# Performance work log

Measured on AMD Instinct MI355X. Metric: run time of the kernel, lower is better.

The kernel has to match this reference:

```python
import jax, jax.numpy as jnp
import numpy as np

N, E, G = 50000, 800000, 512
F, DE, DG = 64, 16, 32
H, HEADS, C, L, NC = 128, 4, 32, 3, 1
EPS = 1e-5


def _bn(x, g, b, m, v):
    # eval-mode BatchNorm1d with running stats
    return (x - m) / jnp.sqrt(v + EPS) * g + b


def setup_inputs():
    key = jax.random.key(0)
    ks = jax.random.split(key, 24)

    def bn_params(k, d):
        k1, k2, k3, k4 = jax.random.split(k, 4)
        return (1.0 + 0.1 * jax.random.normal(k1, (d,), jnp.float32),
                0.1 * jax.random.normal(k2, (d,), jnp.float32),
                0.1 * jax.random.normal(k3, (d,), jnp.float32),
                jax.random.uniform(k4, (d,), jnp.float32, 0.5, 1.5))

    sc = lambda k, sh, fan: jax.random.normal(k, sh, jnp.float32) / np.float32(np.sqrt(fan))
    inp = {}
    inp['x'] = jax.random.normal(ks[0], (N, F), jnp.float32)
    inp['edge_attr'] = jax.random.normal(ks[1], (E, DE), jnp.float32)
    inp['global_features'] = jax.random.normal(ks[2], (G, DG), jnp.float32)
    inp['edge_index'] = jax.random.randint(ks[3], (2, E), 0, N)
    inp['batch'] = jnp.sort(jax.random.randint(ks[4], (N,), 0, G))
    inp['node_w'] = sc(ks[5], (F, H), F); inp['node_b'] = jnp.zeros((H,), jnp.float32)
    inp['node_bn_g'], inp['node_bn_b'], inp['node_bn_m'], inp['node_bn_v'] = bn_params(ks[6], H)
    inp['edge_w'] = sc(ks[7], (DE, H), DE); inp['edge_b'] = jnp.zeros((H,), jnp.float32)
    inp['glob_w'] = sc(ks[8], (DG, H), DG); inp['glob_b'] = jnp.zeros((H,), jnp.float32)
    inp['glob_bn_g'], inp['glob_bn_b'], inp['glob_bn_m'], inp['glob_bn_v'] = bn_params(ks[9], H)
    inp['gat_lin'] = sc(ks[10], (L, H, HEADS * C), H)
    inp['gat_asrc'] = sc(ks[11], (L, HEADS, C), C)
    inp['gat_adst'] = sc(ks[12], (L, HEADS, C), C)
    inp['gat_bias'] = jnp.zeros((L, H), jnp.float32)
    bg, bb, bm, bv = zip(*[bn_params(jax.random.fold_in(ks[13], i), H) for i in range(L)])
    inp['bn_g'] = jnp.stack(bg); inp['bn_b'] = jnp.stack(bb)
    inp['bn_m'] = jnp.stack(bm); inp['bn_v'] = jnp.stack(bv)
    inp['lin1_w'] = sc(ks[14], (3 * H, H), 3 * H); inp['lin1_b'] = jnp.zeros((H,), jnp.float32)
    inp['lin2_w'] = sc(ks[15], (H, NC), H); inp['lin2_b'] = jnp.zeros((NC,), jnp.float32)
    return inp


def reference(x, edge_attr, global_features, edge_index, batch, node_w, node_b, node_bn_g, node_bn_b, node_bn_m, node_bn_v, edge_w, edge_b, glob_w, glob_b, glob_bn_g, glob_bn_b, glob_bn_m, glob_bn_v, gat_lin, gat_asrc, gat_adst, gat_bias, bn_g, bn_b, bn_m, bn_v, lin1_w, lin1_b, lin2_w, lin2_b):
    n = x.shape[0]
    h = jax.nn.relu(_bn(x @ node_w + node_b, node_bn_g, node_bn_b, node_bn_m, node_bn_v))
    _ = jax.nn.relu(edge_attr @ edge_w + edge_b)  # edge encoder: computed but unused by GATConv, as in source
    # add self loops (PyG GATConv default)
    loops = jnp.arange(n)
    src = jnp.concatenate([edge_index[0], loops])
    dst = jnp.concatenate([edge_index[1], loops])
    for i in range(L):
        identity = h
        hh = (h @ gat_lin[i]).reshape(n, HEADS, C)
        a_src = jnp.einsum('nhc,hc->nh', hh, gat_asrc[i])
        a_dst = jnp.einsum('nhc,hc->nh', hh, gat_adst[i])
        e = jax.nn.leaky_relu(a_src[src] + a_dst[dst], 0.2)  # [E+n, HEADS]
        e_max = jax.ops.segment_max(e, dst, num_segments=n)
        ee = jnp.exp(e - e_max[dst])
        den = jax.ops.segment_sum(ee, dst, num_segments=n)
        alpha = ee / (den[dst] + 1e-16)
        out = jax.ops.segment_sum(hh[src] * alpha[..., None], dst, num_segments=n)
        out = out.reshape(n, HEADS * C) + gat_bias[i]
        out = jax.nn.relu(_bn(out, bn_g[i], bn_b[i], bn_m[i], bn_v[i]))
        h = out + identity  # residual: dims always match (HEADS*C == H)
    g = global_features.shape[0]
    cnt = jax.ops.segment_sum(jnp.ones((n,), h.dtype), batch, num_segments=g)
    x_mean = jax.ops.segment_sum(h, batch, num_segments=g) / jnp.maximum(cnt, 1.0)[:, None]
    x_max = jax.ops.segment_max(h, batch, num_segments=g)
    x_max = jnp.where(jnp.isfinite(x_max), x_max, 0.0)  # guard rare empty graphs
    gfeat = jax.nn.relu(_bn(global_features @ glob_w + glob_b, glob_bn_g, glob_bn_b, glob_bn_m, glob_bn_v))
    z = jnp.concatenate([x_mean, x_max, gfeat], axis=1)
    z = jax.nn.relu(z @ lin1_w + lin1_b)
    return z @ lin2_w + lin2_b
```

## Files before the change

### kernel.cpp

```cpp
#include <hip/hip_runtime.h>
#include <hip/hip_bf16.h>

typedef unsigned short u16;
typedef unsigned int   u32;
typedef unsigned long long u64;

#define HD 128
#define FD 64
#define EPS 1e-5f
#define BSH 8
#define CAP 8192
#define TILE 2048

using bf16x8 = __attribute__((ext_vector_type(8))) short;
using f32x4  = __attribute__((ext_vector_type(4))) float;

__device__ __forceinline__ float b2f(u16 v) { return __uint_as_float(((u32)v) << 16); }
__device__ __forceinline__ u16 f2b(float f) {
    u32 u = __float_as_uint(f);
    return (u16)((u + 0x7FFF + ((u >> 16) & 1)) >> 16);
}
__device__ __forceinline__ float lo16(u32 u) { return __uint_as_float(u << 16); }
__device__ __forceinline__ float hi16(u32 u) { return __uint_as_float(u & 0xFFFF0000u); }

__global__ __launch_bounds__(256) void k_prep(
    const float* __restrict__ node_w, const float* __restrict__ gat_lin,
    u16* __restrict__ wf_node, u16* __restrict__ wf_gat,
    const int* __restrict__ batch, int* __restrict__ gs,
    int* __restrict__ zbase, int zn, int N, int G) {
    int y = blockIdx.y;
    int tid = threadIdx.x;
    if (y < 4) {
        const float* src; u16* dst; int K;
        if (y == 0) { src = node_w; dst = wf_node; K = FD; }
        else { src = gat_lin + (size_t)(y - 1) * HD * HD; dst = wf_gat + (size_t)(y - 1) * HD * HD; K = HD; }
        int KT = K >> 5;
        int total = K * HD;
        for (int f = blockIdx.x * 256 + tid; f < total; f += gridDim.x * 256) {
            int j = f & 7;
            int lane = (f >> 3) & 63;
            int t = f >> 9;
            int kt = t % KT;
            int ct = t / KT;
            int k = kt * 32 + (lane >> 4) * 8 + j;
            int col = ct * 16 + (lane & 15);
            dst[f] = f2b(src[k * HD + col]);
        }
    } else if (y == 4) {
        int i = blockIdx.x * 256 + tid;
        if (i < N) {
            int b = batch[i];
            if (i == 0) { for (int g = 0; g <= b; g++) gs[g] = 0; }
            else {
                int pb = batch[i - 1];
                for (int g = pb + 1; g <= b; g++) gs[g] = i;
            }
            if (i == N - 1) { for (int g = b + 1; g <= G; g++) gs[g] = N; }
        }
    } else {
        for (int i = blockIdx.x * 256 + tid; i < zn; i += gridDim.x * 256) zbase[i] = 0;
    }
}

__global__ __launch_bounds__(256) void k_binA_node(
    const int* __restrict__ src, const int* __restrict__ dst,
    int* __restrict__ bcur, u64* __restrict__ arena,
    const float* __restrict__ x, const u16* __restrict__ wf, const float* __restrict__ bias,
    const float* __restrict__ g, const float* __restrict__ bb, const float* __restrict__ m,
    const float* __restrict__ v, u16* __restrict__ h,
    int E, int NB, int numTiles, int N) {
    __shared__ __align__(16) char smem[TILE * 8 + 4 * 256 * 4];
    int tid = threadIdx.x;
    if ((int)blockIdx.x < numTiles) {
        u32* os   = (u32*)smem;
        u32* od   = os + TILE;
        int* hist = (int*)(od + TILE);
        int* obas = hist + 256;
        int* ofs  = obas + 256;
        int* gpos = ofs + 256;
        int base = blockIdx.x * TILE;
        int cntE = E - base; if (cntE > TILE) cntE = TILE;
        hist[tid] = 0;
        __syncthreads();
        u32 rs[TILE / 256], rd[TILE / 256];
        #pragma unroll
        for (int r = 0; r < TILE / 256; r++) {
            int li = r * 256 + tid;
            if (li < cntE) {
                rs[r] = src[base + li];
                rd[r] = dst[base + li];
                atomicAdd(&hist[rd[r] >> BSH], 1);
            }
        }
        __syncthreads();
        if (tid < 64) {
            int h0 = hist[4 * tid], h1 = hist[4 * tid + 1];
            int h2 = hist[4 * tid + 2], h3 = hist[4 * tid + 3];
            int s01 = h0 + h1;
            int loc = s01 + h2 + h3;
            int inc = loc;
            #pragma unroll
            for (int off = 1; off < 64; off <<= 1) {
                int tv = __shfl_up(inc, off);
                if (tid >= off) inc += tv;
            }
            int excl = inc - loc;
            obas[4 * tid] = excl;                 ofs[4 * tid] = excl;
            obas[4 * tid + 1] = excl + h0;        ofs[4 * tid + 1] = excl + h0;
            obas[4 * tid + 2] = excl + s01;       ofs[4 * tid + 2] = excl + s01;
            obas[4 * tid + 3] = excl + s01 + h2;  ofs[4 * tid + 3] = excl + s01 + h2;
        }
        __syncthreads();
        #pragma unroll
        for (int r = 0; r < TILE / 256; r++) {
            int li = r * 256 + tid;
            if (li < cntE) {
                int b = rd[r] >> BSH;
                int posn = atomicAdd(&ofs[b], 1);
                os[posn] = rs[r];
                od[posn] = rd[r];
            }
        }
        __syncthreads();
        if (tid < NB && hist[tid] > 0)
            gpos[tid] = atomicAdd(&bcur[tid], hist[tid]);
        __syncthreads();
        for (int li = tid; li < cntE; li += 256) {
            u32 d = od[li];
            int b = d >> BSH;
            int p = gpos[b] + (li - obas[b]);
            if (p < CAP) arena[(size_t)b * CAP + p] = ((u64)d << 32) | os[li];
        }
    } else {
        int nb = blockIdx.x - numTiles;
        int wv = tid >> 6, lane = tid & 63;
        int rowbase = nb * 64 + wv * 16;
        if (rowbase >= N) return;
        int n16 = lane & 15, quad = lane >> 4;
        int arow = min(rowbase + n16, N - 1);
        f32x4 acc[8] = {};
        #pragma unroll
        for (int kt = 0; kt < 2; kt++) {
            const float4* xp = (const float4*)(x + (size_t)arow * FD + kt * 32 + quad * 8);
            float4 a0 = xp[0], a1 = xp[1];
            bf16x8 a;
            a[0] = (short)f2b(a0.x); a[1] = (short)f2b(a0.y);
            a[2] = (short)f2b(a0.z); a[3] = (short)f2b(a0.w);
            a[4] = (short)f2b(a1.x); a[5] = (short)f2b(a1.y);
            a[6] = (short)f2b(a1.z); a[7] = (short)f2b(a1.w);
            #pragma unroll
            for (int ct = 0; ct < 8; ct++) {
                bf16x8 b = *(const bf16x8*)(wf + ((size_t)(ct * 2 + kt) * 64 + lane) * 8);
                acc[ct] = __builtin_amdgcn_mfma_f32_16x16x32_bf16(a, b, acc[ct], 0, 0, 0);
            }
        }
        #pragma unroll
        for (int ct = 0; ct < 8; ct++) {
            int col = ct * 16 + n16;
            float sc = g[col] * rsqrtf(v[col] + EPS);
            float bi = (bias[col] - m[col]) * sc + bb[col];
            #pragma unroll
            for (int reg = 0; reg < 4; reg++) {
                int row = rowbase + quad * 4 + reg;
                if (row < N) h[(size_t)row * HD + col] = f2b(fmaxf(acc[ct][reg] * sc + bi, 0.f));
            }
        }
    }
}

__global__ __launch_bounds__(256) void k_scanS(const int* __restrict__ bcur, int* __restrict__ bbase, int NB) {
    __shared__ int s[256];
    int tid = threadIdx.x;
    int v = (tid < NB) ? bcur[tid] : 0;
    s[tid] = v;
    __syncthreads();
    for (int off = 1; off < 256; off <<= 1) {
        int t = (tid >= off) ? s[tid - off] : 0;
        __syncthreads();
        s[tid] += t;
        __syncthreads();
    }
    if (tid < NB) bbase[tid] = s[tid] - v;
}

__global__ __launch_bounds__(256) void k_binB2(
    const int* __restrict__ bbase, const int* __restrict__ bcur,
    const u64* __restrict__ arena, int* __restrict__ rowptr, int* __restrict__ colidx,
    int N, int E) {
    __shared__ int rowL[256], lofs[256];
    int b = blockIdx.x, tid = threadIdx.x;
    int n0 = b << BSH;
    int n = n0 + tid;
    int nedge = bcur[b];
    if (nedge > CAP) nedge = CAP;
    lofs[tid] = 0;
    __syncthreads();
    for (int i = tid; i < nedge; i += 256) {
        int d = (int)(arena[(size_t)b * CAP + i] >> 32);
        atomicAdd(&lofs[d - n0], 1);
    }
    __syncthreads();
    rowL[tid] = lofs[tid];
    __syncthreads();
    if (tid < 64) {
        int h0 = rowL[4 * tid], h1 = rowL[4 * tid + 1];
        int h2 = rowL[4 * tid + 2], h3 = rowL[4 * tid + 3];
        int s01 = h0 + h1;
        int loc = s01 + h2 + h3;
        int inc = loc;
        #pragma unroll
        for (int off = 1; off < 64; off <<= 1) {
            int tv = __shfl_up(inc, off);
            if (tid >= off) inc += tv;
        }
        int excl = inc - loc;
        rowL[4 * tid] = excl;
        rowL[4 * tid + 1] = excl + h0;
        rowL[4 * tid + 2] = excl + s01;
        rowL[4 * tid + 3] = excl + s01 + h2;
    }
    __syncthreads();
    int base = bbase[b];
    if (n < N) rowptr[n] = base + rowL[tid];
    if (b == 0 && tid == 0) rowptr[N] = E;
    rowL[tid] += base;
    lofs[tid] = 0;
    __syncthreads();
    for (int i = tid; i < nedge; i += 256) {
        u64 pk = arena[(size_t)b * CAP + i];
        int d = (int)(pk >> 32), s = (int)(pk & 0xFFFFFFFFu);
        int slot = atomicAdd(&lofs[d - n0], 1);
        colidx[rowL[d - n0] + slot] = s;
    }
}

__global__ __launch_bounds__(256) void k_gat_mfma(
    const u16* __restrict__ h, const u16* __restrict__ wf,
    const float* __restrict__ asrcw, const float* __restrict__ adstw,
    u16* __restrict__ hh, float* __restrict__ a_src, float* __restrict__ a_dst, int N) {
    int wv = threadIdx.x >> 6, lane = threadIdx.x & 63;
    int rowbase = blockIdx.x * 64 + wv * 16;
    if (rowbase >= N) return;
    int n16 = lane & 15, quad = lane >> 4;
    int arow = min(rowbase + n16, N - 1);
    f32x4 acc[8] = {};
    #pragma unroll
    for (int kt = 0; kt < 4; kt++) {
        bf16x8 a = *(const bf16x8*)(h + (size_t)arow * HD + kt * 32 + quad * 8);
        #pragma unroll
        for (int ct = 0; ct < 8; ct++) {
            bf16x8 b = *(const bf16x8*)(wf + ((size_t)(ct * 4 + kt) * 64 + lane) * 8);
            acc[ct] = __builtin_amdgcn_mfma_f32_16x16x32_bf16(a, b, acc[ct], 0, 0, 0);
        }
    }
    float asw[8], adw[8];
    #pragma unroll
    for (int ct = 0; ct < 8; ct++) {
        asw[ct] = asrcw[ct * 16 + n16];
        adw[ct] = adstw[ct * 16 + n16];
    }
    float ps[4][4], pd[4][4];
    #pragma unroll
    for (int hd = 0; hd < 4; hd++)
        #pragma unroll
        for (int reg = 0; reg < 4; reg++) {
            ps[hd][reg] = acc[2 * hd][reg] * asw[2 * hd] + acc[2 * hd + 1][reg] * asw[2 * hd + 1];
            pd[hd][reg] = acc[2 * hd][reg] * adw[2 * hd] + acc[2 * hd + 1][reg] * adw[2 * hd + 1];
        }
    #pragma unroll
    for (int msk = 1; msk < 16; msk <<= 1) {
        #pragma unroll
        for (int hd = 0; hd < 4; hd++)
            #pragma unroll
            for (int reg = 0; reg < 4; reg++) {
                ps[hd][reg] += __shfl_xor(ps[hd][reg], msk);
                pd[hd][reg] += __shfl_xor(pd[hd][reg], msk);
            }
    }
    #pragma unroll
    for (int reg = 0; reg < 4; reg++) {
        int row = rowbase + quad * 4 + reg;
        if (row < N) {
            #pragma unroll
            for (int ct = 0; ct < 8; ct++)
                hh[(size_t)row * HD + ct * 16 + n16] = f2b(acc[ct][reg]);
            if (n16 < 4) {
                float ws = 0.f, wd = 0.f;
                #pragma unroll
                for (int hd = 0; hd < 4; hd++)
                    if (n16 == hd) { ws = ps[hd][reg]; wd = pd[hd][reg]; }
                a_src[row * 4 + n16] = ws;
                a_dst[row * 4 + n16] = wd;
            }
        }
    }
}

__global__ __launch_bounds__(256) void k_agg(
    u16* __restrict__ h, const u32* __restrict__ hh32,
    const float* __restrict__ a_src, const float* __restrict__ a_dst,
    const int* __restrict__ rowptr, const int* __restrict__ colidx,
    const float* __restrict__ bias, const float* __restrict__ bng, const float* __restrict__ bnb,
    const float* __restrict__ bnm, const float* __restrict__ bnv, int N) {
    __shared__ int   sL[4][64];
    __shared__ __align__(16) float eeL[4][64][4];
    int wv = threadIdx.x >> 6, lane = threadIdx.x & 63;
    int node = blockIdx.x * 4 + wv;
    if (node >= N) return;
    int head = lane >> 4;
    const float4* as4p = (const float4*)a_src;
    float4 ad4 = ((const float4*)a_dst)[node];
    float adh = (head == 0) ? ad4.x : (head == 1) ? ad4.y : (head == 2) ? ad4.z : ad4.w;
    float ash = a_src[node * 4 + head];
    float e = ash + adh;
    e = (e > 0.f) ? e : 0.2f * e;
    float ee = __expf(e);
    float den = ee;
    u32 hv = hh32[(size_t)node * 64 + lane];
    float acc0 = ee * lo16(hv), acc1 = ee * hi16(hv);
    int beg = rowptr[node], end = rowptr[node + 1];
    for (int base = beg; base < end; base += 64) {
        int cnt = end - base; if (cnt > 64) cnt = 64;
        int s = 0;
        float4 e4 = {0.f, 0.f, 0.f, 0.f};
        if (lane < cnt) {
            s = colidx[base + lane];
            float4 as4 = as4p[s];
            float t0 = as4.x + ad4.x, t1 = as4.y + ad4.y, t2 = as4.z + ad4.z, t3 = as4.w + ad4.w;
            t0 = (t0 > 0.f) ? t0 : 0.2f * t0; t1 = (t1 > 0.f) ? t1 : 0.2f * t1;
            t2 = (t2 > 0.f) ? t2 : 0.2f * t2; t3 = (t3 > 0.f) ? t3 : 0.2f * t3;
            e4.x = __expf(t0); e4.y = __expf(t1); e4.z = __expf(t2); e4.w = __expf(t3);
        }
        sL[wv][lane] = s;
        ((float4*)eeL[wv][lane])[0] = e4;
        int j = 0;
        for (; j + 8 <= cnt; j += 8) {
            u32 hv2[8]; float w[8];
            #pragma unroll
            for (int q = 0; q < 8; q++) {
                int sj = sL[wv][j + q];
                w[q] = eeL[wv][j + q][head];
                hv2[q] = hh32[(size_t)sj * 64 + lane];
            }
            #pragma unroll
            for (int q = 0; q < 8; q++) {
                den += w[q];
                acc0 += w[q] * lo16(hv2[q]);
                acc1 += w[q] * hi16(hv2[q]);
            }
        }
        for (; j < cnt; j++) {
            int sj = sL[wv][j];
            float w = eeL[wv][j][head];
            u32 hv2 = hh32[(size_t)sj * 64 + lane];
            den += w;
            acc0 += w * lo16(hv2);
            acc1 += w * hi16(hv2);
        }
    }
    float inv = 1.0f / (den + 1e-16f);
    int c0 = lane * 2, c1 = c0 + 1;
    float o0 = acc0 * inv, o1 = acc1 * inv;
    float sc0 = bng[c0] * rsqrtf(bnv[c0] + EPS);
    float sc1 = bng[c1] * rsqrtf(bnv[c1] + EPS);
    o0 = (o0 + bias[c0] - bnm[c0]) * sc0 + bnb[c0];
    o1 = (o1 + bias[c1] - bnm[c1]) * sc1 + bnb[c1];
    o0 = fmaxf(o0, 0.f); o1 = fmaxf(o1, 0.f);
    u32 idv = ((const u32*)h)[(size_t)node * 64 + lane];
    o0 += lo16(idv); o1 += hi16(idv);
    ((u32*)h)[(size_t)node * 64 + lane] = ((u32)f2b(o1) << 16) | f2b(o0);
}

__global__ __launch_bounds__(256) void k_pool(
    const u16* __restrict__ h, const int* __restrict__ gs,
    const float* __restrict__ gf, const float* __restrict__ glob_w, const float* __restrict__ glob_b,
    const float* __restrict__ gbg, const float* __restrict__ gbb,
    const float* __restrict__ gbm, const float* __restrict__ gbv,
    float* __restrict__ z, int N, int G) {
    __shared__ float s0L[4][64], s1L[4][64], m0L[4][64], m1L[4][64];
    int g = blockIdx.x, tid = threadIdx.x;
    int wv = tid >> 6, lane = tid & 63;
    int beg = gs[g], end = gs[g + 1];
    const u32* h32 = (const u32*)h;
    float s0 = 0.f, s1 = 0.f, m0 = -3.4e38f, m1 = -3.4e38f;
    for (int r = beg + wv; r < end; r += 4) {
        u32 pk = h32[(size_t)r * 64 + lane];
        float v0 = lo16(pk), v1 = hi16(pk);
        s0 += v0; s1 += v1;
        m0 = fmaxf(m0, v0); m1 = fmaxf(m1, v1);
    }
    s0L[wv][lane] = s0; s1L[wv][lane] = s1;
    m0L[wv][lane] = m0; m1L[wv][lane] = m1;
    __syncthreads();
    if (tid < 64) {
        float a0 = s0L[0][lane] + s0L[1][lane] + s0L[2][lane] + s0L[3][lane];
        float a1 = s1L[0][lane] + s1L[1][lane] + s1L[2][lane] + s1L[3][lane];
        float x0 = fmaxf(fmaxf(m0L[0][lane], m0L[1][lane]), fmaxf(m0L[2][lane], m0L[3][lane]));
        float x1 = fmaxf(fmaxf(m1L[0][lane], m1L[1][lane]), fmaxf(m1L[2][lane], m1L[3][lane]));
        int cnt = end - beg;
        float inv = 1.0f / (float)(cnt > 0 ? cnt : 1);
        if (cnt == 0) { x0 = 0.f; x1 = 0.f; }
        ((float2*)(z + (size_t)g * 384))[lane] = make_float2(a0 * inv, a1 * inv);
        ((float2*)(z + (size_t)g * 384 + 128))[lane] = make_float2(x0, x1);
    } else if (tid >= 128) {
        int c = tid - 128;
        float acc = glob_b[c];
        #pragma unroll 8
        for (int k = 0; k < 32; k++) acc += gf[g * 32 + k] * glob_w[k * HD + c];
        float sc = gbg[c] * rsqrtf(gbv[c] + EPS);
        acc = (acc - gbm[c]) * sc + gbb[c];
        z[(size_t)g * 384 + 256 + c] = fmaxf(acc, 0.f);
    }
}

__global__ __launch_bounds__(256) void k_lin(
    const float* __restrict__ z, const float* __restrict__ W1, const float* __restrict__ b1,
    const float* __restrict__ W2, const float* __restrict__ b2, float* __restrict__ out, int G) {
    __shared__ float zL[8][384];
    __shared__ float Wc[64][128];
    __shared__ float red[8][128];
    int tid = threadIdx.x;
    int g0 = blockIdx.x * 8;
    int c = tid & 127, half = tid >> 7;
    for (int i = tid; i < 8 * 384; i += 256) {
        int gi = i / 384, kk = i % 384;
        zL[gi][kk] = (g0 + gi < G) ? z[(size_t)(g0 + gi) * 384 + kk] : 0.f;
    }
    float acc0 = 0.f, acc1 = 0.f, acc2 = 0.f, acc3 = 0.f;
    int gb = half * 4;
    for (int ch = 0; ch < 6; ch++) {
        __syncthreads();
        for (int i4 = tid; i4 < 2048; i4 += 256) {
            int flat = i4 * 4;
            int k = flat >> 7, cc = flat & 127;
            *(float4*)&Wc[k][cc] = *(const float4*)&W1[(size_t)(ch * 64 + k) * HD + cc];
        }
        __syncthreads();
        int kb = ch * 64;
        #pragma unroll 4
        for (int k = 0; k < 64; k++) {
            float w = Wc[k][c];
            acc0 += zL[gb + 0][kb + k] * w;
            acc1 += zL[gb + 1][kb + k] * w;
            acc2 += zL[gb + 2][kb + k] * w;
            acc3 += zL[gb + 3][kb + k] * w;
        }
    }
    float b1c = b1[c], w2c = W2[c];
    __syncthreads();
    red[gb + 0][c] = fmaxf(acc0 + b1c, 0.f) * w2c;
    red[gb + 1][c] = fmaxf(acc1 + b1c, 0.f) * w2c;
    red[gb + 2][c] = fmaxf(acc2 + b1c, 0.f) * w2c;
    red[gb + 3][c] = fmaxf(acc3 + b1c, 0.f) * w2c;
    __syncthreads();
    int gr = tid >> 5, l32 = tid & 31;
    float v = red[gr][l32] + red[gr][l32 + 32] + red[gr][l32 + 64] + red[gr][l32 + 96];
    #pragma unroll
    for (int m = 1; m < 32; m <<= 1) v += __shfl_xor(v, m, 32);
    if (l32 == 0 && g0 + gr < G) out[g0 + gr] = v + b2[0];
}

extern "C" void kernel_launch(void* const* d_in, const int* in_sizes, int n_in,
                              void* d_out, int out_size, void* d_ws, size_t ws_size,
                              hipStream_t stream) {
    (void)n_in; (void)out_size; (void)ws_size;
    const float* x        = (const float*)d_in[0];
    const float* gfeat    = (const float*)d_in[2];
    const int*   ei       = (const int*)d_in[3];
    const int*   batch    = (const int*)d_in[4];
    const float* node_w   = (const float*)d_in[5];
    const float* node_b   = (const float*)d_in[6];
    const float* nbg      = (const float*)d_in[7];
    const float* nbb      = (const float*)d_in[8];
    const float* nbm      = (const float*)d_in[9];
    const float* nbv      = (const float*)d_in[10];
    const float* glob_w   = (const float*)d_in[13];
    const float* glob_b   = (const float*)d_in[14];
    const float* gbg      = (const float*)d_in[15];
    const float* gbb      = (const float*)d_in[16];
    const float* gbm      = (const float*)d_in[17];
    const float* gbv      = (const float*)d_in[18];
    const float* gat_lin  = (const float*)d_in[19];
    const float* gat_asrc = (const float*)d_in[20];
    const float* gat_adst = (const float*)d_in[21];
    const float* gat_bias = (const float*)d_in[22];
    const float* bn_g     = (const float*)d_in[23];
    const float* bn_b     = (const float*)d_in[24];
    const float* bn_m     = (const float*)d_in[25];
    const float* bn_v     = (const float*)d_in[26];
    const float* lin1_w   = (const float*)d_in[27];
    const float* lin1_b   = (const float*)d_in[28];
    const float* lin2_w   = (const float*)d_in[29];
    const float* lin2_b   = (const float*)d_in[30];

    const int N = in_sizes[0] / FD;
    const int E = in_sizes[3] / 2;
    const int G = in_sizes[2] / 32;
    const int* srcp = ei;
    const int* dstp = ei + E;
    const int NB = (N + 255) >> BSH;
    const int numTiles = (E + TILE - 1) / TILE;

    char* p = (char*)d_ws;
    auto alloc = [&](size_t bytes) -> char* {
        char* r = p;
        p += (bytes + 255) & ~(size_t)255;
        return r;
    };
    u16*   h       = (u16*)alloc((size_t)N * HD * 2);
    u16*   hh      = (u16*)alloc((size_t)N * HD * 2);
    float* a_src   = (float*)alloc((size_t)N * 4 * 4);
    float* a_dst   = (float*)alloc((size_t)N * 4 * 4);
    int*   rowptr  = (int*)alloc((size_t)(N + 1) * 4);
    char*  zbase   = p;
    int*   bcur    = (int*)alloc(256 * 4);
    int    zn      = (int)((p - zbase) / 4);
    int*   bbase   = (int*)alloc(256 * 4);
    u64*   arena   = (u64*)alloc((size_t)NB * CAP * 8);
    int*   colidx  = (int*)alloc((size_t)E * 4);
    u16*   wf_node = (u16*)alloc((size_t)FD * HD * 2);
    u16*   wf_gat  = (u16*)alloc((size_t)3 * HD * HD * 2);
    float* z       = (float*)alloc((size_t)G * 384 * 4);
    int*   gs      = (int*)alloc((size_t)(G + 1) * 4);

    int SB = (N + 255) / 256;

    k_prep<<<dim3(SB, 6), 256, 0, stream>>>(node_w, gat_lin, wf_node, wf_gat,
                                            batch, gs, (int*)zbase, zn, N, G);
    int nodeBlocks = (N + 63) / 64;
    k_binA_node<<<numTiles + nodeBlocks, 256, 0, stream>>>(
        srcp, dstp, bcur, arena,
        x, wf_node, node_b, nbg, nbb, nbm, nbv, h,
        E, NB, numTiles, N);
    k_scanS<<<1, 256, 0, stream>>>(bcur, bbase, NB);
    k_binB2<<<NB, 256, 0, stream>>>(bbase, bcur, arena, rowptr, colidx, N, E);

    for (int i = 0; i < 3; i++) {
        k_gat_mfma<<<(N + 63) / 64, 256, 0, stream>>>(
            h, wf_gat + (size_t)i * HD * HD,
            gat_asrc + i * HD, gat_adst + i * HD,
            hh, a_src, a_dst, N);
        k_agg<<<(N + 3) / 4, 256, 0, stream>>>(
            h, (const u32*)hh, a_src, a_dst, rowptr, colidx,
            gat_bias + i * HD, bn_g + i * HD, bn_b + i * HD, bn_m + i * HD, bn_v + i * HD, N);
    }

    k_pool<<<G, 256, 0, stream>>>(h, gs, gfeat, glob_w, glob_b, gbg, gbb, gbm, gbv, z, N, G);
    k_lin<<<(G + 7) / 8, 256, 0, stream>>>(z, lin1_w, lin1_b, lin2_w, lin2_b, (float*)d_out, G);
}
```

Before: 387.5 us.

## Split GAT aggregation across two waves per node and fold block scan into binning

The aggregation kernel now uses two waves per destination node, each covering half the 128 features. Within a wave the two 32-lane halves take alternating edges and are combined with a cross-lane shuffle at the end. This doubles the threads working on each node's gather, aiming to expose more memory parallelism in the latency-bound neighbor loads, at the cost of redundant edge-score computation in both waves. Separately, the single-block bucket scan kernel is removed and each binning block recomputes the prefix scan of bucket counts itself, saving one launch at the cost of repeated small scans.

New measurement: 452.1 us. +16.7%, slower.

```diff
diff --git a/kernel.cpp b/kernel.cpp
--- a/kernel.cpp
+++ b/kernel.cpp
@@ -168,27 +168,20 @@
     }
 }
 
-__global__ __launch_bounds__(256) void k_scanS(const int* __restrict__ bcur, int* __restrict__ bbase, int NB) {
-    __shared__ int s[256];
-    int tid = threadIdx.x;
-    int v = (tid < NB) ? bcur[tid] : 0;
-    s[tid] = v;
+__global__ __launch_bounds__(256) void k_binB2(
+    const int* __restrict__ bcur, const u64* __restrict__ arena,
+    int* __restrict__ rowptr, int* __restrict__ colidx, int N, int E, int NB) {
+    __shared__ int rowL[256], lofs[256], bsc[256];
+    int b = blockIdx.x, tid = threadIdx.x;
+    bsc[tid] = (tid < NB) ? bcur[tid] : 0;
     __syncthreads();
     for (int off = 1; off < 256; off <<= 1) {
-        int t = (tid >= off) ? s[tid - off] : 0;
-        __syncthreads();
-        s[tid] += t;
-        __syncthreads();
-    }
-    if (tid < NB) bbase[tid] = s[tid] - v;
-}
-
-__global__ __launch_bounds__(256) void k_binB2(
-    const int* __restrict__ bbase, const int* __restrict__ bcur,
-    const u64* __restrict__ arena, int* __restrict__ rowptr, int* __restrict__ colidx,
-    int N, int E) {
-    __shared__ int rowL[256], lofs[256];
-    int b = blockIdx.x, tid = threadIdx.x;
+        int t = (tid >= off) ? bsc[tid - off] : 0;
+        __syncthreads();
+        bsc[tid] += t;
+        __syncthreads();
+    }
+    int base = (b == 0) ? 0 : bsc[b - 1];
     int n0 = b << BSH;
     int n = n0 + tid;
     int nedge = bcur[b];
@@ -220,7 +213,6 @@
         rowL[4 * tid + 3] = excl + s01 + h2;
     }
     __syncthreads();
-    int base = bbase[b];
     if (n < N) rowptr[n] = base + rowL[tid];
     if (b == 0 && tid == 0) rowptr[N] = E;
     rowL[tid] += base;
@@ -296,79 +288,90 @@
     }
 }
 
-__global__ __launch_bounds__(256) void k_agg(
+__global__ __launch_bounds__(512) void k_agg(
     u16* __restrict__ h, const u32* __restrict__ hh32,
     const float* __restrict__ a_src, const float* __restrict__ a_dst,
     const int* __restrict__ rowptr, const int* __restrict__ colidx,
     const float* __restrict__ bias, const float* __restrict__ bng, const float* __restrict__ bnb,
     const float* __restrict__ bnm, const float* __restrict__ bnv, int N) {
-    __shared__ int   sL[4][64];
-    __shared__ __align__(16) float eeL[4][64][4];
-    int wv = threadIdx.x >> 6, lane = threadIdx.x & 63;
-    int node = blockIdx.x * 4 + wv;
+    __shared__ int   sL[8][64];
+    __shared__ __align__(16) float eeL[8][64][4];
+    int tid = threadIdx.x;
+    int wv = tid >> 6, lane = tid & 63;
+    int slot = wv >> 1, halfsel = wv & 1;
+    int node = blockIdx.x * 4 + slot;
     if (node >= N) return;
-    int head = lane >> 4;
-    const float4* as4p = (const float4*)a_src;
+    int l32 = lane & 31, par = lane >> 5;
+    int f = halfsel * 32 + l32;
+    int head = f >> 4;
     float4 ad4 = ((const float4*)a_dst)[node];
     float adh = (head == 0) ? ad4.x : (head == 1) ? ad4.y : (head == 2) ? ad4.z : ad4.w;
-    float ash = a_src[node * 4 + head];
-    float e = ash + adh;
-    e = (e > 0.f) ? e : 0.2f * e;
-    float ee = __expf(e);
-    float den = ee;
-    u32 hv = hh32[(size_t)node * 64 + lane];
-    float acc0 = ee * lo16(hv), acc1 = ee * hi16(hv);
+    float den, acc0, acc1;
+    {
+        float e = a_src[node * 4 + head] + adh;
+        e = (e > 0.f) ? e : 0.2f * e;
+        float ee = __expf(e);
+        if (par == 0) {
+            u32 hv = hh32[(size_t)node * 64 + f];
+            den = ee; acc0 = ee * lo16(hv); acc1 = ee * hi16(hv);
+        } else { den = 0.f; acc0 = 0.f; acc1 = 0.f; }
+    }
+    const float4* as4p = (const float4*)a_src;
     int beg = rowptr[node], end = rowptr[node + 1];
     for (int base = beg; base < end; base += 64) {
         int cnt = end - base; if (cnt > 64) cnt = 64;
-        int s = 0;
-        float4 e4 = {0.f, 0.f, 0.f, 0.f};
         if (lane < cnt) {
-            s = colidx[base + lane];
+            int s = colidx[base + lane];
             float4 as4 = as4p[s];
             float t0 = as4.x + ad4.x, t1 = as4.y + ad4.y, t2 = as4.z + ad4.z, t3 = as4.w + ad4.w;
             t0 = (t0 > 0.f) ? t0 : 0.2f * t0; t1 = (t1 > 0.f) ? t1 : 0.2f * t1;
             t2 = (t2 > 0.f) ? t2 : 0.2f * t2; t3 = (t3 > 0.f) ? t3 : 0.2f * t3;
-            e4.x = __expf(t0); e4.y = __expf(t1); e4.z = __expf(t2); e4.w = __expf(t3);
-        }
-        sL[wv][lane] = s;
-        ((float4*)eeL[wv][lane])[0] = e4;
-        int j = 0;
-        for (; j + 8 <= cnt; j += 8) {
-            u32 hv2[8]; float w[8];
-            #pragma unroll
-            for (int q = 0; q < 8; q++) {
-                int sj = sL[wv][j + q];
-                w[q] = eeL[wv][j + q][head];
-                hv2[q] = hh32[(size_t)sj * 64 + lane];
-            }
-            #pragma unroll
-            for (int q = 0; q < 8; q++) {
+            float4 e4 = { __expf(t0), __expf(t1), __expf(t2), __expf(t3) };
+            sL[wv][lane] = s;
+            ((float4*)eeL[wv][lane])[0] = e4;
+        }
+        int jb = 0;
+        for (; jb + 8 <= cnt; jb += 8) {
+            int sj[4]; float w[4]; u32 hv2[4];
+            #pragma unroll
+            for (int q = 0; q < 4; q++) {
+                int jj = jb + 2 * q + par;
+                sj[q] = sL[wv][jj];
+                w[q]  = eeL[wv][jj][head];
+                hv2[q] = hh32[(size_t)sj[q] * 64 + f];
+            }
+            #pragma unroll
+            for (int q = 0; q < 4; q++) {
                 den += w[q];
                 acc0 += w[q] * lo16(hv2[q]);
                 acc1 += w[q] * hi16(hv2[q]);
             }
         }
-        for (; j < cnt; j++) {
-            int sj = sL[wv][j];
-            float w = eeL[wv][j][head];
-            u32 hv2 = hh32[(size_t)sj * 64 + lane];
+        for (int jj = jb + par; jj < cnt; jj += 2) {
+            int sjv = sL[wv][jj];
+            float w = eeL[wv][jj][head];
+            u32 hv2 = hh32[(size_t)sjv * 64 + f];
             den += w;
             acc0 += w * lo16(hv2);
             acc1 += w * hi16(hv2);
         }
     }
-    float inv = 1.0f / (den + 1e-16f);
-    int c0 = lane * 2, c1 = c0 + 1;
-    float o0 = acc0 * inv, o1 = acc1 * inv;
-    float sc0 = bng[c0] * rsqrtf(bnv[c0] + EPS);
-    float sc1 = bng[c1] * rsqrtf(bnv[c1] + EPS);
-    o0 = (o0 + bias[c0] - bnm[c0]) * sc0 + bnb[c0];
-    o1 = (o1 + bias[c1] - bnm[c1]) * sc1 + bnb[c1];
-    o0 = fmaxf(o0, 0.f); o1 = fmaxf(o1, 0.f);
-    u32 idv = ((const u32*)h)[(size_t)node * 64 + lane];
-    o0 += lo16(idv); o1 += hi16(idv);
-    ((u32*)h)[(size_t)node * 64 + lane] = ((u32)f2b(o1) << 16) | f2b(o0);
+    den  += __shfl_xor(den, 32);
+    acc0 += __shfl_xor(acc0, 32);
+    acc1 += __shfl_xor(acc1, 32);
+    if (par == 0) {
+        float inv = 1.0f / (den + 1e-16f);
+        int c0 = f * 2, c1 = c0 + 1;
+        float o0 = acc0 * inv, o1 = acc1 * inv;
+        float sc0 = bng[c0] * rsqrtf(bnv[c0] + EPS);
+        float sc1 = bng[c1] * rsqrtf(bnv[c1] + EPS);
+        o0 = (o0 + bias[c0] - bnm[c0]) * sc0 + bnb[c0];
+        o1 = (o1 + bias[c1] - bnm[c1]) * sc1 + bnb[c1];
+        o0 = fmaxf(o0, 0.f); o1 = fmaxf(o1, 0.f);
+        u32 idv = ((const u32*)h)[(size_t)node * 64 + f];
+        o0 += lo16(idv); o1 += hi16(idv);
+        ((u32*)h)[(size_t)node * 64 + f] = ((u32)f2b(o1) << 16) | f2b(o0);
+    }
 }
 
 __global__ __launch_bounds__(256) void k_pool(
@@ -515,7 +518,6 @@
     char*  zbase   = p;
     int*   bcur    = (int*)alloc(256 * 4);
     int    zn      = (int)((p - zbase) / 4);
-    int*   bbase   = (int*)alloc(256 * 4);
     u64*   arena   = (u64*)alloc((size_t)NB * CAP * 8);
     int*   colidx  = (int*)alloc((size_t)E * 4);
     u16*   wf_node = (u16*)alloc((size_t)FD * HD * 2);
@@ -532,15 +534,14 @@
         srcp, dstp, bcur, arena,
         x, wf_node, node_b, nbg, nbb, nbm, nbv, h,
         E, NB, numTiles, N);
-    k_scanS<<<1, 256, 0, stream>>>(bcur, bbase, NB);
-    k_binB2<<<NB, 256, 0, stream>>>(bbase, bcur, arena, rowptr, colidx, N, E);
+    k_binB2<<<NB, 256, 0, stream>>>(bcur, arena, rowptr, colidx, N, E, NB);
 
     for (int i = 0; i < 3; i++) {
         k_gat_mfma<<<(N + 63) / 64, 256, 0, stream>>>(
             h, wf_gat + (size_t)i * HD * HD,
             gat_asrc + i * HD, gat_adst + i * HD,
             hh, a_src, a_dst, N);
-        k_agg<<<(N + 3) / 4, 256, 0, stream>>>(
+        k_agg<<<(N + 3) / 4, 512, 0, stream>>>(
             h, (const u32*)hh, a_src, a_dst, rowptr, colidx,
             gat_bias + i * HD, bn_g + i * HD, bn_b + i * HD, bn_m + i * HD, bn_v + i * HD, N);
     }
```
